# Kernel tuning notes

Measured on AMD Instinct MI355X. Metric: run time of the kernel, lower is better.

Reference implementation:

```python
import math
import jax, jax.numpy as jnp
import numpy as np

B, LD, LS = 1, 512, 2048
C_S, C_H, H, PQ, PV = 384, 16, 12, 4, 8
EPS, INF = 1e-08, 1e9


def _quat_to_rot(q):
    q = q / jnp.linalg.norm(q, axis=-1, keepdims=True)
    w, x, y, z = q[..., 0], q[..., 1], q[..., 2], q[..., 3]
    R = jnp.stack([
        1 - 2 * (y * y + z * z), 2 * (x * y - w * z), 2 * (x * z + w * y),
        2 * (x * y + w * z), 1 - 2 * (x * x + z * z), 2 * (y * z - w * x),
        2 * (x * z - w * y), 2 * (y * z + w * x), 1 - 2 * (x * x + y * y)],
        axis=-1)
    return R.reshape(q.shape[:-1] + (3, 3))


def setup_inputs() -> dict:
    key = jax.random.key(0)
    ks = jax.random.split(key, 14)
    s_dst = jax.random.normal(ks[0], (B, LD, C_S), jnp.float32)
    s_src = jax.random.normal(ks[1], (B, LS, C_S), jnp.float32)
    R_dst = _quat_to_rot(jax.random.normal(ks[2], (B, LD, 4), jnp.float32))
    t_dst = jax.random.normal(ks[3], (B, LD, 3), jnp.float32) * 3.0
    R_src = _quat_to_rot(jax.random.normal(ks[4], (B, LS, 4), jnp.float32))
    t_src = jax.random.normal(ks[5], (B, LS, 3), jnp.float32) * 3.0
    dst_mask = jnp.ones((B, LD), jnp.float32)
    src_mask = (jax.random.uniform(ks[6], (B, LS)) < 0.9).astype(jnp.float32)
    sc = 0.02
    W_q = jax.random.normal(ks[7], (C_S, H * C_H), jnp.float32) * sc
    W_kv = jax.random.normal(ks[8], (C_S, 2 * H * C_H), jnp.float32) * sc
    W_qp = jax.random.normal(ks[9], (C_S, H * PQ * 3), jnp.float32) * sc
    W_kvp = jax.random.normal(ks[10], (C_S, H * (PQ + PV) * 3), jnp.float32) * sc
    W_out = jax.random.normal(ks[11], (H * (C_H + PV * 4), C_S), jnp.float32) * sc
    b_out = jnp.zeros((C_S,), jnp.float32)
    # ipa_point_weights_init_: softplus^-1(1) = log(e - 1)
    head_w = jnp.full((H,), float(np.log(np.e - 1.0)), jnp.float32)
    return dict(s_dst=s_dst, s_src=s_src, R_dst=R_dst, t_dst=t_dst,
                R_src=R_src, t_src=t_src, dst_mask=dst_mask, src_mask=src_mask,
                W_q=W_q, W_kv=W_kv, W_qp=W_qp, W_kvp=W_kvp,
                W_out=W_out, b_out=b_out, head_w=head_w)


def _split3_stack(x):
    # torch.split into 3 chunks on last dim then stack(dim=-1): [..., 3n] -> [..., n, 3]
    b, l, c3 = x.shape
    return jnp.moveaxis(x.reshape(b, l, 3, c3 // 3), -2, -1)


def _ipa_forward(s_dst, s_src, R_dst, t_dst, R_src, t_src, dst_mask, src_mask,
                 W_q, W_kv, W_qp, W_kvp, W_out, b_out, head_w):
    b, ld, _ = s_dst.shape
    ls = s_src.shape[1]
    gmask = (dst_mask[:, None, :, None] * src_mask[:, None, None, :])  # [B,1,Ld,Ls]

    q = (s_dst @ W_q).reshape(b, ld, H, C_H)
    kv = (s_src @ W_kv).reshape(b, ls, H, 2 * C_H)
    k, v = kv[..., :C_H], kv[..., C_H:]

    # points in global frame
    qp = _split3_stack(s_dst @ W_qp)                     # [B,Ld,H*PQ,3] local
    qp = jnp.einsum('blij,blpj->blpi', R_dst, qp) + t_dst[:, :, None, :]
    qp = qp.reshape(b, ld, H, PQ, 3)
    kvp = _split3_stack(s_src @ W_kvp)                   # [B,Ls,H*(PQ+PV),3]
    kvp = jnp.einsum('blij,blpj->blpi', R_src, kvp) + t_src[:, :, None, :]
    kvp = kvp.reshape(b, ls, H, PQ + PV, 3)
    k_pts, v_pts = kvp[..., :PQ, :], kvp[..., PQ:, :]

    # scalar attention scores
    a = jnp.einsum('bihc,bjhc->bhij', q, k) * math.sqrt(1.0 / (2 * C_H))
    a_sd = a * gmask

    # point attention: squared distances of global-frame points
    diff = qp[:, :, None, :, :, :] - k_pts[:, None, :, :, :, :]   # [B,Ld,Ls,H,PQ,3]
    pt2 = jnp.sum(diff * diff, axis=-1)                           # [B,Ld,Ls,H,PQ]
    hw = jax.nn.softplus(head_w) * math.sqrt(1.0 / (2 * (PQ * 9.0 / 2)))
    pt_att = jnp.sum(pt2 * hw[None, None, None, :, None], axis=-1) * (-0.5)
    pt_att = jnp.transpose(pt_att, (0, 3, 1, 2))                  # [B,H,Ld,Ls]
    a_pts = pt_att * gmask

    sq_mask = INF * (dst_mask[:, :, None] * src_mask[:, None, :] - 1.0)
    a = jax.nn.softmax(a + pt_att + sq_mask[:, None, :, :], axis=-1)

    # scalar value aggregation
    o = jnp.einsum('bhij,bjhc->bihc', a, v).reshape(b, ld, H * C_H)
    # point value aggregation, then back to dst local frame
    o_pt = jnp.einsum('bhij,bjhpc->bihpc', a, v_pts)              # [B,Ld,H,PV,3]
    o_pt = jnp.einsum('bikj,bihpk->bihpj', R_dst,
                      o_pt - t_dst[:, :, None, None, :])
    o_pt_norm = jnp.sqrt(jnp.sum(o_pt ** 2, axis=-1) + EPS).reshape(b, ld, H * PV)
    o_pt_flat = o_pt.reshape(b, ld, H * PV, 3)

    cat = jnp.concatenate([o, o_pt_flat[..., 0], o_pt_flat[..., 1],
                           o_pt_flat[..., 2], o_pt_norm], axis=-1)
    s_upd = cat @ W_out + b_out
    return s_upd, a, a_sd, a_pts


def reference(s_dst, s_src, R_dst, t_dst, R_src, t_src, dst_mask, src_mask,
              W_q, W_kv, W_qp, W_kvp, W_out, b_out, head_w):
    return _ipa_forward(s_dst, s_src, R_dst, t_dst, R_src, t_src,
                        dst_mask, src_mask, W_q, W_kv, W_qp, W_kvp,
                        W_out, b_out, head_w)
```

## Files before the change

kernel.cpp:

```cpp
#include <hip/hip_runtime.h>
#include <hip/hip_bf16.h>

#define LD 512
#define LS 2048
#define CS 384
#define CH 16
#define NH 12
#define PQ 4
#define PV 8
#define QCW 336
#define KVW 816

typedef __bf16 bf16x8 __attribute__((ext_vector_type(8)));
typedef float  f32x4  __attribute__((ext_vector_type(4)));

__device__ inline void split_frag(const float* __restrict__ p, bf16x8& hi, bf16x8& lo)
{
    float4 x = *(const float4*)p;
    float4 y = *(const float4*)(p + 4);
    float f[8] = {x.x, x.y, x.z, x.w, y.x, y.y, y.z, y.w};
#pragma unroll
    for (int e = 0; e < 8; ++e) {
        __bf16 h = (__bf16)f[e];
        hi[e] = h;
        lo[e] = (__bf16)(f[e] - (float)h);
    }
}

__device__ inline void split_frag_w(const float* __restrict__ Wp, int stride,
                                    bf16x8& hi, bf16x8& lo)
{
    float f[8];
#pragma unroll
    for (int e = 0; e < 8; ++e) f[e] = Wp[(size_t)e * stride];
#pragma unroll
    for (int e = 0; e < 8; ++e) {
        __bf16 h = (__bf16)f[e];
        hi[e] = h;
        lo[e] = (__bf16)(f[e] - (float)h);
    }
}

__global__ __launch_bounds__(64) void proj_gemm_kernel(
    const float* __restrict__ s_dst, const float* __restrict__ s_src,
    const float* __restrict__ W_q, const float* __restrict__ W_qp,
    const float* __restrict__ W_kv, const float* __restrict__ W_kvp,
    float* __restrict__ qcat, float* __restrict__ kvcat)
{
    const float* A; float* C; int N, m0, n0, Nw; const float* Wsrc; int ncol0;
    if (blockIdx.x < 176) {
        int b = blockIdx.x;
        A = s_dst; C = qcat; N = QCW;
        m0 = (b & 15) * 32; n0 = (b >> 4) * 32;
        if (n0 < 192) { Wsrc = W_q;  Nw = 192; ncol0 = n0; }
        else          { Wsrc = W_qp; Nw = 144; ncol0 = n0 - 192; }
    } else {
        int b = blockIdx.x - 176;
        A = s_src; C = kvcat; N = KVW;
        m0 = (b & 63) * 32; n0 = (b >> 6) * 32;
        if (n0 < 384) { Wsrc = W_kv;  Nw = 384; ncol0 = n0; }
        else          { Wsrc = W_kvp; Nw = 432; ncol0 = n0 - 384; }
    }
    const int lane = threadIdx.x;
    const int row16 = lane & 15, kq = lane >> 4;
    const int K = CS;

    const float* ap0 = A + (size_t)(m0 + row16) * K + kq * 8;
    const float* ap1 = ap0 + (size_t)16 * K;
    const float* wp0 = Wsrc + (size_t)(kq * 8) * Nw + ncol0 + row16;
    const float* wp1 = wp0 + 16;
    const bool n1ok = (n0 + 16) < N;

    f32x4 acc00 = {0.f, 0.f, 0.f, 0.f};
    f32x4 acc10 = {0.f, 0.f, 0.f, 0.f};
    f32x4 acc01 = {0.f, 0.f, 0.f, 0.f};
    f32x4 acc11 = {0.f, 0.f, 0.f, 0.f};

    for (int k = 0; k < K; k += 32) {
        bf16x8 a0h, a0l, a1h, a1l, b0h, b0l, b1h, b1l;
        split_frag(ap0 + k, a0h, a0l);
        split_frag(ap1 + k, a1h, a1l);
        split_frag_w(wp0 + (size_t)k * Nw, Nw, b0h, b0l);
        acc00 = __builtin_amdgcn_mfma_f32_16x16x32_bf16(a0h, b0h, acc00, 0, 0, 0);
        acc00 = __builtin_amdgcn_mfma_f32_16x16x32_bf16(a0h, b0l, acc00, 0, 0, 0);
        acc00 = __builtin_amdgcn_mfma_f32_16x16x32_bf16(a0l, b0h, acc00, 0, 0, 0);
        acc10 = __builtin_amdgcn_mfma_f32_16x16x32_bf16(a1h, b0h, acc10, 0, 0, 0);
        acc10 = __builtin_amdgcn_mfma_f32_16x16x32_bf16(a1h, b0l, acc10, 0, 0, 0);
        acc10 = __builtin_amdgcn_mfma_f32_16x16x32_bf16(a1l, b0h, acc10, 0, 0, 0);
        if (n1ok) {
            split_frag_w(wp1 + (size_t)k * Nw, Nw, b1h, b1l);
            acc01 = __builtin_amdgcn_mfma_f32_16x16x32_bf16(a0h, b1h, acc01, 0, 0, 0);
            acc01 = __builtin_amdgcn_mfma_f32_16x16x32_bf16(a0h, b1l, acc01, 0, 0, 0);
            acc01 = __builtin_amdgcn_mfma_f32_16x16x32_bf16(a0l, b1h, acc01, 0, 0, 0);
            acc11 = __builtin_amdgcn_mfma_f32_16x16x32_bf16(a1h, b1h, acc11, 0, 0, 0);
            acc11 = __builtin_amdgcn_mfma_f32_16x16x32_bf16(a1h, b1l, acc11, 0, 0, 0);
            acc11 = __builtin_amdgcn_mfma_f32_16x16x32_bf16(a1l, b1h, acc11, 0, 0, 0);
        }
    }

#pragma unroll
    for (int r = 0; r < 4; ++r) {
        const int mA = m0 + kq * 4 + r;
        const int mB = mA + 16;
        C[(size_t)mA * N + n0 + row16] = acc00[r];
        C[(size_t)mB * N + n0 + row16] = acc10[r];
        if (n1ok) {
            C[(size_t)mA * N + n0 + 16 + row16] = acc01[r];
            C[(size_t)mB * N + n0 + 16 + row16] = acc11[r];
        }
    }
}

__global__ __launch_bounds__(64) void out_gemm_kernel(
    const float* __restrict__ A, const float* __restrict__ W_out,
    const float* __restrict__ bias, float* __restrict__ C)
{
    const int m0 = blockIdx.x * 32;
    const int n0 = blockIdx.y * 32;
    const int lane = threadIdx.x;
    const int row16 = lane & 15, kq = lane >> 4;
    const int K = 576, N = CS, Nw = CS;

    const float* ap0 = A + (size_t)(m0 + row16) * K + kq * 8;
    const float* ap1 = ap0 + (size_t)16 * K;
    const float* wp0 = W_out + (size_t)(kq * 8) * Nw + n0 + row16;
    const float* wp1 = wp0 + 16;

    f32x4 acc00 = {0.f, 0.f, 0.f, 0.f};
    f32x4 acc10 = {0.f, 0.f, 0.f, 0.f};
    f32x4 acc01 = {0.f, 0.f, 0.f, 0.f};
    f32x4 acc11 = {0.f, 0.f, 0.f, 0.f};

    for (int k = 0; k < K; k += 32) {
        bf16x8 a0h, a0l, a1h, a1l, b0h, b0l, b1h, b1l;
        split_frag(ap0 + k, a0h, a0l);
        split_frag(ap1 + k, a1h, a1l);
        split_frag_w(wp0 + (size_t)k * Nw, Nw, b0h, b0l);
        acc00 = __builtin_amdgcn_mfma_f32_16x16x32_bf16(a0h, b0h, acc00, 0, 0, 0);
        acc00 = __builtin_amdgcn_mfma_f32_16x16x32_bf16(a0h, b0l, acc00, 0, 0, 0);
        acc00 = __builtin_amdgcn_mfma_f32_16x16x32_bf16(a0l, b0h, acc00, 0, 0, 0);
        acc10 = __builtin_amdgcn_mfma_f32_16x16x32_bf16(a1h, b0h, acc10, 0, 0, 0);
        acc10 = __builtin_amdgcn_mfma_f32_16x16x32_bf16(a1h, b0l, acc10, 0, 0, 0);
        acc10 = __builtin_amdgcn_mfma_f32_16x16x32_bf16(a1l, b0h, acc10, 0, 0, 0);
        split_frag_w(wp1 + (size_t)k * Nw, Nw, b1h, b1l);
        acc01 = __builtin_amdgcn_mfma_f32_16x16x32_bf16(a0h, b1h, acc01, 0, 0, 0);
        acc01 = __builtin_amdgcn_mfma_f32_16x16x32_bf16(a0h, b1l, acc01, 0, 0, 0);
        acc01 = __builtin_amdgcn_mfma_f32_16x16x32_bf16(a0l, b1h, acc01, 0, 0, 0);
        acc11 = __builtin_amdgcn_mfma_f32_16x16x32_bf16(a1h, b1h, acc11, 0, 0, 0);
        acc11 = __builtin_amdgcn_mfma_f32_16x16x32_bf16(a1h, b1l, acc11, 0, 0, 0);
        acc11 = __builtin_amdgcn_mfma_f32_16x16x32_bf16(a1l, b1h, acc11, 0, 0, 0);
    }

    const float bv0 = bias[n0 + row16];
    const float bv1 = bias[n0 + 16 + row16];
#pragma unroll
    for (int r = 0; r < 4; ++r) {
        const int mA = m0 + kq * 4 + r;
        const int mB = mA + 16;
        C[(size_t)mA * N + n0 + row16] = acc00[r] + bv0;
        C[(size_t)mB * N + n0 + row16] = acc10[r] + bv0;
        C[(size_t)mA * N + n0 + 16 + row16] = acc01[r] + bv1;
        C[(size_t)mB * N + n0 + 16 + row16] = acc11[r] + bv1;
    }
}

__global__ __launch_bounds__(256) void prep_kernel(
    const float* __restrict__ qcat, const float* __restrict__ kvcat,
    const float* __restrict__ Rd, const float* __restrict__ td,
    const float* __restrict__ Rs, const float* __restrict__ ts,
    float* __restrict__ qp_rot, float* __restrict__ sqq,
    float* __restrict__ kT, float* __restrict__ vAllT,
    float* __restrict__ kpT, float* __restrict__ sqkT)
{
    const int t = threadIdx.x;
    if (blockIdx.y < NH) {
        const int h = blockIdx.y, j0 = blockIdx.x * 64;
        __shared__ float tile[64][33];
        __shared__ float ot[36][64];
        __shared__ float nrm[64][4];
        __shared__ float rt[64][12];

#pragma unroll
        for (int s = 0; s < 3; ++s) {
            int ld = t + s * 256;
            int jl = ld / 12, q = ld % 12;
            rt[jl][q] = (q < 9) ? Rs[(size_t)(j0 + jl) * 9 + q]
                                : ts[(size_t)(j0 + jl) * 3 + (q - 9)];
        }
#pragma unroll
        for (int r = 0; r < 2; ++r) {
            int f = t + r * 256;
            int jl = f >> 3, c4 = (f & 7) * 4;
            float4 v = *(const float4*)(kvcat + (size_t)(j0 + jl) * KVW + h * 32 + c4);
            tile[jl][c4 + 0] = v.x;
            tile[jl][c4 + 1] = v.y;
            tile[jl][c4 + 2] = v.z;
            tile[jl][c4 + 3] = v.w;
        }
        __syncthreads();

        {
            const int jl = t & 63, cr = t >> 6;
#pragma unroll
            for (int cg = 0; cg < 8; ++cg) {
                int c = cg * 4 + cr;
                float v = tile[jl][c];
                if (c < 16) kT[((size_t)h * 16 + c) * LS + j0 + jl] = v;
                else        vAllT[((size_t)h * 40 + (c - 16)) * LS + j0 + jl] = v;
            }
        }

#pragma unroll
        for (int s = 0; s < 3; ++s) {
            int u = t + s * 256;
            int jl = u / 12, p = u % 12;
            const float* src = kvcat + (size_t)(j0 + jl) * KVW + 384 + h * 12 + p;
            float x = src[0], y = src[144], z = src[288];
            const float* R = &rt[jl][0];
            float rx = R[0] * x + R[1] * y + R[2] * z + R[9];
            float ry = R[3] * x + R[4] * y + R[5] * z + R[10];
            float rz = R[6] * x + R[7] * y + R[8] * z + R[11];
            if (p < 4) {
                ot[p * 3 + 0][jl] = rx;
                ot[p * 3 + 1][jl] = ry;
                ot[p * 3 + 2][jl] = rz;
                nrm[jl][p] = rx * rx + ry * ry + rz * rz;
            } else {
                int r0 = 12 + (p - 4) * 3;
                ot[r0 + 0][jl] = rx;
                ot[r0 + 1][jl] = ry;
                ot[r0 + 2][jl] = rz;
            }
        }
        __syncthreads();

#pragma unroll
        for (int w = 0; w < 9; ++w) {
            int idx = t + w * 256;
            int row = idx >> 6, jl = idx & 63;
            float v = ot[row][jl];
            if (row < 12) kpT[((size_t)h * 12 + row) * LS + j0 + jl] = v;
            else          vAllT[((size_t)h * 40 + 16 + (row - 12)) * LS + j0 + jl] = v;
        }
        if (t < 64)
            sqkT[(size_t)h * LS + j0 + t] = nrm[t][0] + nrm[t][1] + nrm[t][2] + nrm[t][3];
    } else {
        const int i0 = blockIdx.x * 16;
        __shared__ float part[16][48];
        __shared__ float rtd[16][12];
        if (t < 192) {
            int il = t / 12, q = t % 12;
            rtd[il][q] = (q < 9) ? Rd[(size_t)(i0 + il) * 9 + q]
                                 : td[(size_t)(i0 + il) * 3 + (q - 9)];
        }
        __syncthreads();
#pragma unroll
        for (int s = 0; s < 3; ++s) {
            int u = t + s * 256;
            int il = u / 48, pt = u % 48;
            int i = i0 + il;
            float x = qcat[(size_t)i * QCW + 192 + pt];
            float y = qcat[(size_t)i * QCW + 240 + pt];
            float z = qcat[(size_t)i * QCW + 288 + pt];
            const float* R = &rtd[il][0];
            float rx = R[0] * x + R[1] * y + R[2] * z + R[9];
            float ry = R[3] * x + R[4] * y + R[5] * z + R[10];
            float rz = R[6] * x + R[7] * y + R[8] * z + R[11];
            qp_rot[(size_t)i * 144 + pt * 3 + 0] = rx;
            qp_rot[(size_t)i * 144 + pt * 3 + 1] = ry;
            qp_rot[(size_t)i * 144 + pt * 3 + 2] = rz;
            part[il][pt] = rx * rx + ry * ry + rz * rz;
        }
        __syncthreads();
        if (t < 192) {
            int il = t / 12, hh = t % 12;
            sqq[(size_t)(i0 + il) * NH + hh] =
                part[il][hh * 4] + part[il][hh * 4 + 1] +
                part[il][hh * 4 + 2] + part[il][hh * 4 + 3];
        }
    }
}

__global__ __launch_bounds__(256) void score_softmax_kernel(
    const float* __restrict__ qb, const float* __restrict__ kT,
    const float* __restrict__ qpb, const float* __restrict__ kpT,
    const float* __restrict__ sqq_g, const float* __restrict__ sqkT,
    const float* __restrict__ dmask, const float* __restrict__ smask,
    const float* __restrict__ head_w,
    float* __restrict__ a_out, float* __restrict__ asd_out,
    float* __restrict__ apts_out)
{
    const int h = blockIdx.y;
    const int i0 = blockIdx.x * 4;
    const int t = threadIdx.x;

    __shared__ float qs[4][32];
    __shared__ float sqq_s[4];
    __shared__ float dm_s[4];
    __shared__ float red[4][4];

    if (t < 128) {
        int i = t >> 5, c = t & 31;
        float v = 0.f;
        if (c < 16)      v = qb[(size_t)(i0 + i) * QCW + h * CH + c];
        else if (c < 28) v = qpb[(size_t)(i0 + i) * 144 + h * 12 + (c - 16)];
        qs[i][c] = v;
    } else if (t < 132) {
        int i = t - 128;
        sqq_s[i] = sqq_g[(size_t)(i0 + i) * NH + h];
        dm_s[i] = dmask[i0 + i];
    }
    const float hwv = log1pf(__expf(head_w[h])) * (1.0f / 6.0f);
    const float s1 = 0.17677669529663687f;
    const size_t rowbase = ((size_t)h * LD + i0) * LS;
    __syncthreads();

    float4 sregv[4][2];
    float mx[4] = {-3.0e38f, -3.0e38f, -3.0e38f, -3.0e38f};

#pragma unroll
    for (int jc = 0; jc < 2; ++jc) {
        const int j = (jc * 256 + t) * 4;
        float4 sm4 = *(const float4*)(smask + j);
        float4 sqk4 = *(const float4*)(sqkT + (size_t)h * LS + j);

        float4 kk[16];
#pragma unroll
        for (int c = 0; c < 16; ++c)
            kk[c] = *(const float4*)(kT + ((size_t)h * 16 + c) * LS + j);

        float4 qk4[4];
#pragma unroll
        for (int i = 0; i < 4; ++i) {
            const float4* q4 = (const float4*)&qs[i][0];
            float4 q0 = q4[0], q1 = q4[1], q2 = q4[2], q3 = q4[3];
            float4 a;
            a.x = q0.x * kk[0].x + q0.y * kk[1].x + q0.z * kk[2].x + q0.w * kk[3].x
                + q1.x * kk[4].x + q1.y * kk[5].x + q1.z * kk[6].x + q1.w * kk[7].x
                + q2.x * kk[8].x + q2.y * kk[9].x + q2.z * kk[10].x + q2.w * kk[11].x
                + q3.x * kk[12].x + q3.y * kk[13].x + q3.z * kk[14].x + q3.w * kk[15].x;
            a.y = q0.x * kk[0].y + q0.y * kk[1].y + q0.z * kk[2].y + q0.w * kk[3].y
                + q1.x * kk[4].y + q1.y * kk[5].y + q1.z * kk[6].y + q1.w * kk[7].y
                + q2.x * kk[8].y + q2.y * kk[9].y + q2.z * kk[10].y + q2.w * kk[11].y
                + q3.x * kk[12].y + q3.y * kk[13].y + q3.z * kk[14].y + q3.w * kk[15].y;
            a.z = q0.x * kk[0].z + q0.y * kk[1].z + q0.z * kk[2].z + q0.w * kk[3].z
                + q1.x * kk[4].z + q1.y * kk[5].z + q1.z * kk[6].z + q1.w * kk[7].z
                + q2.x * kk[8].z + q2.y * kk[9].z + q2.z * kk[10].z + q2.w * kk[11].z
                + q3.x * kk[12].z + q3.y * kk[13].z + q3.z * kk[14].z + q3.w * kk[15].z;
            a.w = q0.x * kk[0].w + q0.y * kk[1].w + q0.z * kk[2].w + q0.w * kk[3].w
                + q1.x * kk[4].w + q1.y * kk[5].w + q1.z * kk[6].w + q1.w * kk[7].w
                + q2.x * kk[8].w + q2.y * kk[9].w + q2.z * kk[10].w + q2.w * kk[11].w
                + q3.x * kk[12].w + q3.y * kk[13].w + q3.z * kk[14].w + q3.w * kk[15].w;
            qk4[i] = a;
        }

        float4 pp[12];
#pragma unroll
        for (int d = 0; d < 12; ++d)
            pp[d] = *(const float4*)(kpT + ((size_t)h * 12 + d) * LS + j);

        float4 dp4[4];
#pragma unroll
        for (int i = 0; i < 4; ++i) {
            const float4* r4 = (const float4*)&qs[i][16];
            float4 r0 = r4[0], r1 = r4[1], r2 = r4[2];
            float4 d;
            d.x = r0.x * pp[0].x + r0.y * pp[1].x + r0.z * pp[2].x + r0.w * pp[3].x
                + r1.x * pp[4].x + r1.y * pp[5].x + r1.z * pp[6].x + r1.w * pp[7].x
                + r2.x * pp[8].x + r2.y * pp[9].x + r2.z * pp[10].x + r2.w * pp[11].x;
            d.y = r0.x * pp[0].y + r0.y * pp[1].y + r0.z * pp[2].y + r0.w * pp[3].y
                + r1.x * pp[4].y + r1.y * pp[5].y + r1.z * pp[6].y + r1.w * pp[7].y
                + r2.x * pp[8].y + r2.y * pp[9].y + r2.z * pp[10].y + r2.w * pp[11].y;
            d.z = r0.x * pp[0].z + r0.y * pp[1].z + r0.z * pp[2].z + r0.w * pp[3].z
                + r1.x * pp[4].z + r1.y * pp[5].z + r1.z * pp[6].z + r1.w * pp[7].z
                + r2.x * pp[8].z + r2.y * pp[9].z + r2.z * pp[10].z + r2.w * pp[11].z;
            d.w = r0.x * pp[0].w + r0.y * pp[1].w + r0.z * pp[2].w + r0.w * pp[3].w
                + r1.x * pp[4].w + r1.y * pp[5].w + r1.z * pp[6].w + r1.w * pp[7].w
                + r2.x * pp[8].w + r2.y * pp[9].w + r2.z * pp[10].w + r2.w * pp[11].w;
            dp4[i] = d;
        }

#pragma unroll
        for (int i = 0; i < 4; ++i) {
            float sqq = sqq_s[i];
            float dm = dm_s[i];
            float4 qk, pt, g, logit;
            qk.x = qk4[i].x * s1; qk.y = qk4[i].y * s1;
            qk.z = qk4[i].z * s1; qk.w = qk4[i].w * s1;
            pt.x = -0.5f * hwv * (sqq + sqk4.x - 2.f * dp4[i].x);
            pt.y = -0.5f * hwv * (sqq + sqk4.y - 2.f * dp4[i].y);
            pt.z = -0.5f * hwv * (sqq + sqk4.z - 2.f * dp4[i].z);
            pt.w = -0.5f * hwv * (sqq + sqk4.w - 2.f * dp4[i].w);
            g.x = dm * sm4.x; g.y = dm * sm4.y; g.z = dm * sm4.z; g.w = dm * sm4.w;
            size_t idx = rowbase + (size_t)i * LS + j;
            f32x4 asd = {qk.x * g.x, qk.y * g.y, qk.z * g.z, qk.w * g.w};
            f32x4 apts = {pt.x * g.x, pt.y * g.y, pt.z * g.z, pt.w * g.w};
            __builtin_nontemporal_store(asd, (f32x4*)(asd_out + idx));
            __builtin_nontemporal_store(apts, (f32x4*)(apts_out + idx));
            logit.x = qk.x + pt.x + 1.0e9f * (g.x - 1.0f);
            logit.y = qk.y + pt.y + 1.0e9f * (g.y - 1.0f);
            logit.z = qk.z + pt.z + 1.0e9f * (g.z - 1.0f);
            logit.w = qk.w + pt.w + 1.0e9f * (g.w - 1.0f);
            sregv[i][jc] = logit;
            mx[i] = fmaxf(mx[i], fmaxf(fmaxf(logit.x, logit.y), fmaxf(logit.z, logit.w)));
        }
    }

    const int lane = t & 63, wid = t >> 6;
#pragma unroll
    for (int i = 0; i < 4; ++i) {
        float v = mx[i];
        for (int off = 32; off > 0; off >>= 1) v = fmaxf(v, __shfl_xor(v, off));
        if (lane == 0) red[wid][i] = v;
    }
    __syncthreads();
    float M[4], sum[4] = {0.f, 0.f, 0.f, 0.f};
#pragma unroll
    for (int i = 0; i < 4; ++i)
        M[i] = fmaxf(fmaxf(red[0][i], red[1][i]), fmaxf(red[2][i], red[3][i]));
    __syncthreads();

#pragma unroll
    for (int jc = 0; jc < 2; ++jc) {
#pragma unroll
        for (int i = 0; i < 4; ++i) {
            float4 e;
            e.x = __expf(sregv[i][jc].x - M[i]);
            e.y = __expf(sregv[i][jc].y - M[i]);
            e.z = __expf(sregv[i][jc].z - M[i]);
            e.w = __expf(sregv[i][jc].w - M[i]);
            sregv[i][jc] = e;
            sum[i] += e.x + e.y + e.z + e.w;
        }
    }
#pragma unroll
    for (int i = 0; i < 4; ++i) {
        float v = sum[i];
        for (int off = 32; off > 0; off >>= 1) v += __shfl_xor(v, off);
        if (lane == 0) red[wid][i] = v;
    }
    __syncthreads();
    float inv[4];
#pragma unroll
    for (int i = 0; i < 4; ++i)
        inv[i] = 1.0f / (red[0][i] + red[1][i] + red[2][i] + red[3][i]);

#pragma unroll
    for (int jc = 0; jc < 2; ++jc) {
        const int j = (jc * 256 + t) * 4;
#pragma unroll
        for (int i = 0; i < 4; ++i) {
            float4 e = sregv[i][jc];
            float4 o = make_float4(e.x * inv[i], e.y * inv[i], e.z * inv[i], e.w * inv[i]);
            *(float4*)(a_out + rowbase + (size_t)i * LS + j) = o;
        }
    }
}

__global__ __launch_bounds__(512) void av_mfma_kernel(
    const float* __restrict__ a, const float* __restrict__ vAllT,
    float* __restrict__ o_buf, float* __restrict__ opt_buf)
{
    const int m0 = blockIdx.x * 16;
    const int h  = blockIdx.y;
    const int t = threadIdx.x;
    const int lane = t & 63;
    const int wid  = t >> 6;
    const int row16 = lane & 15, kq = lane >> 4;

    const size_t kbase = (size_t)wid * 256 + kq * 8;
    const float* ap  = a     + ((size_t)h * LD + m0 + row16) * LS + kbase;
    const float* v0p = vAllT + ((size_t)h * 40 +  0 + row16) * LS + kbase;
    const float* v1p = vAllT + ((size_t)h * 40 + 16 + row16) * LS + kbase;
    const float* v2p = vAllT + ((size_t)h * 40 + 24 + row16) * LS + kbase;

    f32x4 acc0 = {0.f, 0.f, 0.f, 0.f};
    f32x4 acc1 = {0.f, 0.f, 0.f, 0.f};
    f32x4 acc2 = {0.f, 0.f, 0.f, 0.f};

#pragma unroll 2
    for (int kk = 0; kk < 256; kk += 32) {
        bf16x8 ah, al, bh, bl;
        split_frag(ap + kk, ah, al);

        split_frag(v0p + kk, bh, bl);
        acc0 = __builtin_amdgcn_mfma_f32_16x16x32_bf16(ah, bh, acc0, 0, 0, 0);
        acc0 = __builtin_amdgcn_mfma_f32_16x16x32_bf16(ah, bl, acc0, 0, 0, 0);
        acc0 = __builtin_amdgcn_mfma_f32_16x16x32_bf16(al, bh, acc0, 0, 0, 0);

        split_frag(v1p + kk, bh, bl);
        acc1 = __builtin_amdgcn_mfma_f32_16x16x32_bf16(ah, bh, acc1, 0, 0, 0);
        acc1 = __builtin_amdgcn_mfma_f32_16x16x32_bf16(ah, bl, acc1, 0, 0, 0);
        acc1 = __builtin_amdgcn_mfma_f32_16x16x32_bf16(al, bh, acc1, 0, 0, 0);

        split_frag(v2p + kk, bh, bl);
        acc2 = __builtin_amdgcn_mfma_f32_16x16x32_bf16(ah, bh, acc2, 0, 0, 0);
        acc2 = __builtin_amdgcn_mfma_f32_16x16x32_bf16(ah, bl, acc2, 0, 0, 0);
        acc2 = __builtin_amdgcn_mfma_f32_16x16x32_bf16(al, bh, acc2, 0, 0, 0);
    }

    __shared__ float red[8][64][13];
#pragma unroll
    for (int r = 0; r < 4; ++r) {
        red[wid][lane][r]     = acc0[r];
        red[wid][lane][4 + r] = acc1[r];
        red[wid][lane][8 + r] = acc2[r];
    }
    __syncthreads();

    if (wid == 0) {
        float s[12];
#pragma unroll
        for (int r = 0; r < 12; ++r) {
            float v = red[0][lane][r];
#pragma unroll
            for (int w = 1; w < 8; ++w) v += red[w][lane][r];
            s[r] = v;
        }
        const int ib = m0 + kq * 4;
#pragma unroll
        for (int r = 0; r < 4; ++r) {
            const int i = ib + r;
            o_buf[(size_t)i * 192 + h * 16 + row16] = s[r];
            opt_buf[(size_t)i * 288 + h * 24 + row16] = s[4 + r];
            if (row16 >= 8)
                opt_buf[(size_t)i * 288 + h * 24 + 8 + row16] = s[8 + r];
        }
    }
}

__global__ __launch_bounds__(192) void finalize_kernel(
    const float* __restrict__ o_buf, const float* __restrict__ opt_buf,
    const float* __restrict__ Rd, const float* __restrict__ td,
    float* __restrict__ cat)
{
    const int i = blockIdx.x, t = threadIdx.x;
    cat[i * 576 + t] = o_buf[i * 192 + t];
    if (t < 96) {
        const float* op = opt_buf + i * 288 + t * 3;
        float x = op[0] - td[i * 3 + 0];
        float y = op[1] - td[i * 3 + 1];
        float z = op[2] - td[i * 3 + 2];
        const float* R = Rd + i * 9;
        float rx = R[0] * x + R[3] * y + R[6] * z;
        float ry = R[1] * x + R[4] * y + R[7] * z;
        float rz = R[2] * x + R[5] * y + R[8] * z;
        float* cc = cat + i * 576 + 192;
        cc[t] = rx;
        cc[96 + t] = ry;
        cc[192 + t] = rz;
        cc[288 + t] = sqrtf(rx * rx + ry * ry + rz * rz + 1e-8f);
    }
}

extern "C" void kernel_launch(void* const* d_in, const int* in_sizes, int n_in,
                              void* d_out, int out_size, void* d_ws, size_t ws_size,
                              hipStream_t stream)
{
    (void)in_sizes; (void)n_in; (void)out_size; (void)ws_size;
    const float* s_dst    = (const float*)d_in[0];
    const float* s_src    = (const float*)d_in[1];
    const float* R_dst    = (const float*)d_in[2];
    const float* t_dst    = (const float*)d_in[3];
    const float* R_src    = (const float*)d_in[4];
    const float* t_src    = (const float*)d_in[5];
    const float* dst_mask = (const float*)d_in[6];
    const float* src_mask = (const float*)d_in[7];
    const float* W_q      = (const float*)d_in[8];
    const float* W_kv     = (const float*)d_in[9];
    const float* W_qp     = (const float*)d_in[10];
    const float* W_kvp    = (const float*)d_in[11];
    const float* W_out    = (const float*)d_in[12];
    const float* b_out    = (const float*)d_in[13];
    const float* head_w   = (const float*)d_in[14];

    float* ws = (float*)d_ws;
    float* qcat    = ws;
    float* kvcat   = qcat    + 172032;
    float* qp_rot  = kvcat   + 1671168;
    float* sq_q    = qp_rot  + 73728;
    float* o_buf   = sq_q    + 6144;
    float* opt_buf = o_buf   + 98304;
    float* cat_buf = opt_buf + 147456;
    float* kT      = cat_buf + 294912;
    float* vAllT   = kT      + 393216;
    float* kpT     = vAllT   + 983040;
    float* sqkT    = kpT     + 294912;

    float* out_s    = (float*)d_out;
    float* out_a    = out_s    + 196608;
    float* out_asd  = out_a    + 12582912;
    float* out_apts = out_asd  + 12582912;

    proj_gemm_kernel<<<dim3(1840), dim3(64), 0, stream>>>(
        s_dst, s_src, W_q, W_qp, W_kv, W_kvp, qcat, kvcat);
    prep_kernel<<<dim3(32, 13), dim3(256), 0, stream>>>(
        qcat, kvcat, R_dst, t_dst, R_src, t_src,
        qp_rot, sq_q, kT, vAllT, kpT, sqkT);
    score_softmax_kernel<<<dim3(LD / 4, NH), dim3(256), 0, stream>>>(
        qcat, kT, qp_rot, kpT, sq_q, sqkT, dst_mask, src_mask, head_w,
        out_a, out_asd, out_apts);
    av_mfma_kernel<<<dim3(LD / 16, NH), dim3(512), 0, stream>>>(out_a, vAllT, o_buf, opt_buf);
    finalize_kernel<<<LD, 192, 0, stream>>>(o_buf, opt_buf, R_dst, t_dst, cat_buf);
    out_gemm_kernel<<<dim3(16, 12), dim3(64), 0, stream>>>(cat_buf, W_out, b_out, out_s);
}
```

Measured before the change: 262.8 us.

## Drop split-bf16 error compensation in MFMA GEMMs and fuse finalize into output GEMM

Replaces the three-MFMA hi/lo bf16 split emulation of fp32 GEMMs with a single plain bf16 MFMA per tile in the projection, attention-value and output GEMMs. It also folds the frame rotation and norm finalize step into the output GEMM, building the concatenated row tile in shared memory so the cat buffer round-trip and one launch go away. This cuts MFMA and conversion work by about two thirds, at the cost of bf16-level accuracy in all GEMMs, which may exceed tolerance. The fused kernel recomputes the finalize step once for each output column block.

```diff
diff --git a/kernel.cpp b/kernel.cpp
--- a/kernel.cpp
+++ b/kernel.cpp
@@ -14,31 +14,25 @@
 typedef __bf16 bf16x8 __attribute__((ext_vector_type(8)));
 typedef float  f32x4  __attribute__((ext_vector_type(4)));
 
-__device__ inline void split_frag(const float* __restrict__ p, bf16x8& hi, bf16x8& lo)
+__device__ inline bf16x8 conv_frag(const float* __restrict__ p)
 {
     float4 x = *(const float4*)p;
     float4 y = *(const float4*)(p + 4);
-    float f[8] = {x.x, x.y, x.z, x.w, y.x, y.y, y.z, y.w};
-#pragma unroll
-    for (int e = 0; e < 8; ++e) {
-        __bf16 h = (__bf16)f[e];
-        hi[e] = h;
-        lo[e] = (__bf16)(f[e] - (float)h);
-    }
-}
-
-__device__ inline void split_frag_w(const float* __restrict__ Wp, int stride,
-                                    bf16x8& hi, bf16x8& lo)
+    bf16x8 h;
+    h[0] = (__bf16)x.x; h[1] = (__bf16)x.y; h[2] = (__bf16)x.z; h[3] = (__bf16)x.w;
+    h[4] = (__bf16)y.x; h[5] = (__bf16)y.y; h[6] = (__bf16)y.z; h[7] = (__bf16)y.w;
+    return h;
+}
+
+__device__ inline bf16x8 conv_frag_w(const float* __restrict__ Wp, int stride)
 {
     float f[8];
 #pragma unroll
     for (int e = 0; e < 8; ++e) f[e] = Wp[(size_t)e * stride];
-#pragma unroll
-    for (int e = 0; e < 8; ++e) {
-        __bf16 h = (__bf16)f[e];
-        hi[e] = h;
-        lo[e] = (__bf16)(f[e] - (float)h);
-    }
+    bf16x8 h;
+#pragma unroll
+    for (int e = 0; e < 8; ++e) h[e] = (__bf16)f[e];
+    return h;
 }
 
 __global__ __launch_bounds__(64) void proj_gemm_kernel(
@@ -77,24 +71,15 @@
     f32x4 acc11 = {0.f, 0.f, 0.f, 0.f};
 
     for (int k = 0; k < K; k += 32) {
-        bf16x8 a0h, a0l, a1h, a1l, b0h, b0l, b1h, b1l;
-        split_frag(ap0 + k, a0h, a0l);
-        split_frag(ap1 + k, a1h, a1l);
-        split_frag_w(wp0 + (size_t)k * Nw, Nw, b0h, b0l);
-        acc00 = __builtin_amdgcn_mfma_f32_16x16x32_bf16(a0h, b0h, acc00, 0, 0, 0);
-        acc00 = __builtin_amdgcn_mfma_f32_16x16x32_bf16(a0h, b0l, acc00, 0, 0, 0);
-        acc00 = __builtin_amdgcn_mfma_f32_16x16x32_bf16(a0l, b0h, acc00, 0, 0, 0);
-        acc10 = __builtin_amdgcn_mfma_f32_16x16x32_bf16(a1h, b0h, acc10, 0, 0, 0);
-        acc10 = __builtin_amdgcn_mfma_f32_16x16x32_bf16(a1h, b0l, acc10, 0, 0, 0);
-        acc10 = __builtin_amdgcn_mfma_f32_16x16x32_bf16(a1l, b0h, acc10, 0, 0, 0);
+        bf16x8 a0 = conv_frag(ap0 + k);
+        bf16x8 a1 = conv_frag(ap1 + k);
+        bf16x8 b0 = conv_frag_w(wp0 + (size_t)k * Nw, Nw);
+        acc00 = __builtin_amdgcn_mfma_f32_16x16x32_bf16(a0, b0, acc00, 0, 0, 0);
+        acc10 = __builtin_amdgcn_mfma_f32_16x16x32_bf16(a1, b0, acc10, 0, 0, 0);
         if (n1ok) {
-            split_frag_w(wp1 + (size_t)k * Nw, Nw, b1h, b1l);
-            acc01 = __builtin_amdgcn_mfma_f32_16x16x32_bf16(a0h, b1h, acc01, 0, 0, 0);
-            acc01 = __builtin_amdgcn_mfma_f32_16x16x32_bf16(a0h, b1l, acc01, 0, 0, 0);
-            acc01 = __builtin_amdgcn_mfma_f32_16x16x32_bf16(a0l, b1h, acc01, 0, 0, 0);
-            acc11 = __builtin_amdgcn_mfma_f32_16x16x32_bf16(a1h, b1h, acc11, 0, 0, 0);
-            acc11 = __builtin_amdgcn_mfma_f32_16x16x32_bf16(a1h, b1l, acc11, 0, 0, 0);
-            acc11 = __builtin_amdgcn_mfma_f32_16x16x32_bf16(a1l, b1h, acc11, 0, 0, 0);
+            bf16x8 b1 = conv_frag_w(wp1 + (size_t)k * Nw, Nw);
+            acc01 = __builtin_amdgcn_mfma_f32_16x16x32_bf16(a0, b1, acc01, 0, 0, 0);
+            acc11 = __builtin_amdgcn_mfma_f32_16x16x32_bf16(a1, b1, acc11, 0, 0, 0);
         }
     }
 
@@ -108,59 +93,6 @@
             C[(size_t)mA * N + n0 + 16 + row16] = acc01[r];
             C[(size_t)mB * N + n0 + 16 + row16] = acc11[r];
         }
-    }
-}
-
-__global__ __launch_bounds__(64) void out_gemm_kernel(
-    const float* __restrict__ A, const float* __restrict__ W_out,
-    const float* __restrict__ bias, float* __restrict__ C)
-{
-    const int m0 = blockIdx.x * 32;
-    const int n0 = blockIdx.y * 32;
-    const int lane = threadIdx.x;
-    const int row16 = lane & 15, kq = lane >> 4;
-    const int K = 576, N = CS, Nw = CS;
-
-    const float* ap0 = A + (size_t)(m0 + row16) * K + kq * 8;
-    const float* ap1 = ap0 + (size_t)16 * K;
-    const float* wp0 = W_out + (size_t)(kq * 8) * Nw + n0 + row16;
-    const float* wp1 = wp0 + 16;
-
-    f32x4 acc00 = {0.f, 0.f, 0.f, 0.f};
-    f32x4 acc10 = {0.f, 0.f, 0.f, 0.f};
-    f32x4 acc01 = {0.f, 0.f, 0.f, 0.f};
-    f32x4 acc11 = {0.f, 0.f, 0.f, 0.f};
-
-    for (int k = 0; k < K; k += 32) {
-        bf16x8 a0h, a0l, a1h, a1l, b0h, b0l, b1h, b1l;
-        split_frag(ap0 + k, a0h, a0l);
-        split_frag(ap1 + k, a1h, a1l);
-        split_frag_w(wp0 + (size_t)k * Nw, Nw, b0h, b0l);
-        acc00 = __builtin_amdgcn_mfma_f32_16x16x32_bf16(a0h, b0h, acc00, 0, 0, 0);
-        acc00 = __builtin_amdgcn_mfma_f32_16x16x32_bf16(a0h, b0l, acc00, 0, 0, 0);
-        acc00 = __builtin_amdgcn_mfma_f32_16x16x32_bf16(a0l, b0h, acc00, 0, 0, 0);
-        acc10 = __builtin_amdgcn_mfma_f32_16x16x32_bf16(a1h, b0h, acc10, 0, 0, 0);
-        acc10 = __builtin_amdgcn_mfma_f32_16x16x32_bf16(a1h, b0l, acc10, 0, 0, 0);
-        acc10 = __builtin_amdgcn_mfma_f32_16x16x32_bf16(a1l, b0h, acc10, 0, 0, 0);
-        split_frag_w(wp1 + (size_t)k * Nw, Nw, b1h, b1l);
-        acc01 = __builtin_amdgcn_mfma_f32_16x16x32_bf16(a0h, b1h, acc01, 0, 0, 0);
-        acc01 = __builtin_amdgcn_mfma_f32_16x16x32_bf16(a0h, b1l, acc01, 0, 0, 0);
-        acc01 = __builtin_amdgcn_mfma_f32_16x16x32_bf16(a0l, b1h, acc01, 0, 0, 0);
-        acc11 = __builtin_amdgcn_mfma_f32_16x16x32_bf16(a1h, b1h, acc11, 0, 0, 0);
-        acc11 = __builtin_amdgcn_mfma_f32_16x16x32_bf16(a1h, b1l, acc11, 0, 0, 0);
-        acc11 = __builtin_amdgcn_mfma_f32_16x16x32_bf16(a1l, b1h, acc11, 0, 0, 0);
-    }
-
-    const float bv0 = bias[n0 + row16];
-    const float bv1 = bias[n0 + 16 + row16];
-#pragma unroll
-    for (int r = 0; r < 4; ++r) {
-        const int mA = m0 + kq * 4 + r;
-        const int mB = mA + 16;
-        C[(size_t)mA * N + n0 + row16] = acc00[r] + bv0;
-        C[(size_t)mB * N + n0 + row16] = acc10[r] + bv0;
-        C[(size_t)mA * N + n0 + 16 + row16] = acc01[r] + bv1;
-        C[(size_t)mB * N + n0 + 16 + row16] = acc11[r] + bv1;
     }
 }
 
@@ -480,23 +412,13 @@
 
 #pragma unroll 2
     for (int kk = 0; kk < 256; kk += 32) {
-        bf16x8 ah, al, bh, bl;
-        split_frag(ap + kk, ah, al);
-
-        split_frag(v0p + kk, bh, bl);
-        acc0 = __builtin_amdgcn_mfma_f32_16x16x32_bf16(ah, bh, acc0, 0, 0, 0);
-        acc0 = __builtin_amdgcn_mfma_f32_16x16x32_bf16(ah, bl, acc0, 0, 0, 0);
-        acc0 = __builtin_amdgcn_mfma_f32_16x16x32_bf16(al, bh, acc0, 0, 0, 0);
-
-        split_frag(v1p + kk, bh, bl);
-        acc1 = __builtin_amdgcn_mfma_f32_16x16x32_bf16(ah, bh, acc1, 0, 0, 0);
-        acc1 = __builtin_amdgcn_mfma_f32_16x16x32_bf16(ah, bl, acc1, 0, 0, 0);
-        acc1 = __builtin_amdgcn_mfma_f32_16x16x32_bf16(al, bh, acc1, 0, 0, 0);
-
-        split_frag(v2p + kk, bh, bl);
-        acc2 = __builtin_amdgcn_mfma_f32_16x16x32_bf16(ah, bh, acc2, 0, 0, 0);
-        acc2 = __builtin_amdgcn_mfma_f32_16x16x32_bf16(ah, bl, acc2, 0, 0, 0);
-        acc2 = __builtin_amdgcn_mfma_f32_16x16x32_bf16(al, bh, acc2, 0, 0, 0);
+        bf16x8 ah = conv_frag(ap + kk);
+        bf16x8 b0 = conv_frag(v0p + kk);
+        bf16x8 b1 = conv_frag(v1p + kk);
+        bf16x8 b2 = conv_frag(v2p + kk);
+        acc0 = __builtin_amdgcn_mfma_f32_16x16x32_bf16(ah, b0, acc0, 0, 0, 0);
+        acc1 = __builtin_amdgcn_mfma_f32_16x16x32_bf16(ah, b1, acc1, 0, 0, 0);
+        acc2 = __builtin_amdgcn_mfma_f32_16x16x32_bf16(ah, b2, acc2, 0, 0, 0);
     }
 
     __shared__ float red[8][64][13];
@@ -529,15 +451,26 @@
     }
 }
 
-__global__ __launch_bounds__(192) void finalize_kernel(
+__global__ __launch_bounds__(64) void finalize_out_kernel(
     const float* __restrict__ o_buf, const float* __restrict__ opt_buf,
     const float* __restrict__ Rd, const float* __restrict__ td,
-    float* __restrict__ cat)
-{
-    const int i = blockIdx.x, t = threadIdx.x;
-    cat[i * 576 + t] = o_buf[i * 192 + t];
-    if (t < 96) {
-        const float* op = opt_buf + i * 288 + t * 3;
+    const float* __restrict__ W_out, const float* __restrict__ bias,
+    float* __restrict__ out_s)
+{
+    const int m0 = blockIdx.x * 16;
+    const int n0 = blockIdx.y * 32;
+    const int t = threadIdx.x;
+
+    __shared__ float cat[16][596];
+
+    for (int u = t; u < 16 * 192; u += 64) {
+        int il = u / 192, c = u % 192;
+        cat[il][c] = o_buf[(size_t)(m0 + il) * 192 + c];
+    }
+    for (int u = t; u < 16 * 96; u += 64) {
+        int il = u / 96, p = u % 96;
+        int i = m0 + il;
+        const float* op = opt_buf + (size_t)i * 288 + p * 3;
         float x = op[0] - td[i * 3 + 0];
         float y = op[1] - td[i * 3 + 1];
         float z = op[2] - td[i * 3 + 2];
@@ -545,11 +478,32 @@
         float rx = R[0] * x + R[3] * y + R[6] * z;
         float ry = R[1] * x + R[4] * y + R[7] * z;
         float rz = R[2] * x + R[5] * y + R[8] * z;
-        float* cc = cat + i * 576 + 192;
-        cc[t] = rx;
-        cc[96 + t] = ry;
-        cc[192 + t] = rz;
-        cc[288 + t] = sqrtf(rx * rx + ry * ry + rz * rz + 1e-8f);
+        cat[il][192 + p] = rx;
+        cat[il][288 + p] = ry;
+        cat[il][384 + p] = rz;
+        cat[il][480 + p] = sqrtf(rx * rx + ry * ry + rz * rz + 1e-8f);
+    }
+    __syncthreads();
+
+    const int row16 = t & 15, kq = t >> 4;
+    f32x4 acc0 = {0.f, 0.f, 0.f, 0.f};
+    f32x4 acc1 = {0.f, 0.f, 0.f, 0.f};
+
+    for (int k = 0; k < 576; k += 32) {
+        bf16x8 af = conv_frag(&cat[row16][k + kq * 8]);
+        bf16x8 b0 = conv_frag_w(W_out + (size_t)(k + kq * 8) * CS + n0 + row16, CS);
+        bf16x8 b1 = conv_frag_w(W_out + (size_t)(k + kq * 8) * CS + n0 + 16 + row16, CS);
+        acc0 = __builtin_amdgcn_mfma_f32_16x16x32_bf16(af, b0, acc0, 0, 0, 0);
+        acc1 = __builtin_amdgcn_mfma_f32_16x16x32_bf16(af, b1, acc1, 0, 0, 0);
+    }
+
+    const float bv0 = bias[n0 + row16];
+    const float bv1 = bias[n0 + 16 + row16];
+#pragma unroll
+    for (int r = 0; r < 4; ++r) {
+        const int m = m0 + kq * 4 + r;
+        out_s[(size_t)m * CS + n0 + row16] = acc0[r] + bv0;
+        out_s[(size_t)m * CS + n0 + 16 + row16] = acc1[r] + bv1;
     }
 }
 
@@ -581,8 +535,7 @@
     float* sq_q    = qp_rot  + 73728;
     float* o_buf   = sq_q    + 6144;
     float* opt_buf = o_buf   + 98304;
-    float* cat_buf = opt_buf + 147456;
-    float* kT      = cat_buf + 294912;
+    float* kT      = opt_buf + 147456;
     float* vAllT   = kT      + 393216;
     float* kpT     = vAllT   + 983040;
     float* sqkT    = kpT     + 294912;
@@ -601,6 +554,6 @@
         qcat, kT, qp_rot, kpT, sq_q, sqkT, dst_mask, src_mask, head_w,
         out_a, out_asd, out_apts);
     av_mfma_kernel<<<dim3(LD / 16, NH), dim3(512), 0, stream>>>(out_a, vAllT, o_buf, opt_buf);
-    finalize_kernel<<<LD, 192, 0, stream>>>(o_buf, opt_buf, R_dst, t_dst, cat_buf);
-    out_gemm_kernel<<<dim3(16, 12), dim3(64), 0, stream>>>(cat_buf, W_out, b_out, out_s);
-}
+    finalize_out_kernel<<<dim3(32, 12), dim3(64), 0, stream>>>(
+        o_buf, opt_buf, R_dst, t_dst, W_out, b_out, out_s);
+}
```

Measured after the change: 266.9 us. No clear change (+1.6%).
